# Performance work log

Measured on AMD Instinct MI355X. Metric: run time of the kernel, lower is better.

The kernel has to match this reference:

```python
import jax, jax.numpy as jnp
import numpy as np

N_NODES = 100000
N_EDGES = 400000
N_REL = 3
N_LAYERS = 2
D = 128          # input feature dim == hidden_dim so weights stack cleanly
N_CLASSES = 2


def setup_inputs() -> dict:
    key = jax.random.key(0)
    ks = jax.random.split(key, 7)
    x = jax.random.normal(ks[0], (N_NODES, D), dtype=jnp.float32)
    edge_index = jax.random.randint(ks[1], (N_REL, 2, N_EDGES), 0, N_NODES, dtype=jnp.int32)
    # SAGEConv params per (layer, relation): neighbor weight, root weight, bias
    Wn = jax.random.normal(ks[2], (N_LAYERS, N_REL, D, D), dtype=jnp.float32) * (1.0 / np.sqrt(D))
    Wr = jax.random.normal(ks[3], (N_LAYERS, N_REL, D, D), dtype=jnp.float32) * (1.0 / np.sqrt(D))
    b = jax.random.normal(ks[4], (N_LAYERS, N_REL, D), dtype=jnp.float32) * 0.02
    Wc = jax.random.normal(ks[5], (D, N_CLASSES), dtype=jnp.float32) * (1.0 / np.sqrt(D))
    bc = jax.random.normal(ks[6], (N_CLASSES,), dtype=jnp.float32) * 0.02
    return {"x": x, "edge_index": edge_index, "Wn": Wn, "Wr": Wr, "b": b, "Wc": Wc, "bc": bc}


def _mean_agg(h, ei, n_nodes):
    # gather source features, scatter-mean into destination nodes
    src, dst = ei[0], ei[1]
    s = jax.ops.segment_sum(h[src], dst, num_segments=n_nodes)          # [N, D]
    cnt = jax.ops.segment_sum(jnp.ones((ei.shape[1],), h.dtype), dst, num_segments=n_nodes)
    return s / jnp.maximum(cnt, 1.0)[:, None]


def reference(x, edge_index, Wn, Wr, b, Wc, bc):
    n = x.shape[0]
    h = x
    L, R = Wn.shape[0], Wn.shape[1]
    for l in range(L):
        out = jnp.zeros((n, Wn.shape[-1]), h.dtype)
        for r in range(R):
            # SAGEConv: lin_l(mean neighbors) + lin_r(root) + bias; HeteroConv sums relations
            agg = _mean_agg(h, edge_index[r], n)
            out = out + agg @ Wn[l, r] + h @ Wr[l, r] + b[l, r]
        h = jax.nn.relu(out) if l < L - 1 else out  # dropout is eval-mode identity
    return h @ Wc + bc
```

## Files before the change

kernel.cpp:

```cpp
#include <hip/hip_runtime.h>

#define NN 100000
#define NE 400000
#define NR 3
#define DD 128
#define NROWS (NR * NN)
#define NEDGES (NR * NE)
#define SCAN_BLOCKS ((NROWS + 1023) / 1024)

typedef float f32x4 __attribute__((ext_vector_type(4)));
typedef __bf16 bf16x8 __attribute__((ext_vector_type(8)));

__device__ __forceinline__ unsigned short f2bf(float f) {
    unsigned int u = __float_as_uint(f);
    u += 0x7fff + ((u >> 16) & 1);
    return (unsigned short)(u >> 16);
}

__device__ __forceinline__ void gload16(const void* g, void* l) {
    __builtin_amdgcn_global_load_lds(
        (const __attribute__((address_space(1))) void*)g,
        (__attribute__((address_space(3))) void*)l, 16, 0, 0);
}

__global__ __launch_bounds__(256) void cvt_x(const float* __restrict__ x,
                                             unsigned short* __restrict__ xb) {
    int i = blockIdx.x * 256 + threadIdx.x;
    const float4* xf = reinterpret_cast<const float4*>(x + (size_t)i * 8);
    float4 a = xf[0], b = xf[1];
    uint4 o;
    o.x = (unsigned)f2bf(a.x) | ((unsigned)f2bf(a.y) << 16);
    o.y = (unsigned)f2bf(a.z) | ((unsigned)f2bf(a.w) << 16);
    o.z = (unsigned)f2bf(b.x) | ((unsigned)f2bf(b.y) << 16);
    o.w = (unsigned)f2bf(b.z) | ((unsigned)f2bf(b.w) << 16);
    reinterpret_cast<uint4*>(xb)[i] = o;
}

__global__ __launch_bounds__(256) void prep_w(const float* __restrict__ Wn,
                                              const float* __restrict__ Wr,
                                              unsigned short* __restrict__ Wt) {
    int t = blockIdx.x * 256 + threadIdx.x;
    if (t >= 2 * 128 * 512) return;
    int l = t >> 16;
    int rem = t & 65535;
    int n = rem >> 9;
    int k = rem & 511;
    int rk = k >> 7, kk = k & 127;
    float v;
    if (rk < 3) {
        v = Wn[(((size_t)l * 3 + rk) * 128 + kk) * 128 + n];
    } else {
        const float* WrL = Wr + (size_t)l * 3 * 128 * 128;
        v = WrL[kk * 128 + n] + WrL[128 * 128 + kk * 128 + n] + WrL[2 * 128 * 128 + kk * 128 + n];
    }
    Wt[((size_t)l * 128 + n) * 512 + k] = f2bf(v);
}

__global__ __launch_bounds__(256) void prep_b(const float* __restrict__ b,
                                              float* __restrict__ bias) {
    int t = threadIdx.x;
    int l = t >> 7, n = t & 127;
    bias[t] = b[l * 384 + n] + b[l * 384 + 128 + n] + b[l * 384 + 256 + n];
}

__global__ __launch_bounds__(256) void csr_count(const int* __restrict__ ei,
                                                 int* __restrict__ cnt) {
    int t = blockIdx.x * 256 + threadIdx.x;
    if (t >= NEDGES) return;
    int r = t / NE;
    int e = t - r * NE;
    int dst = ei[(r * 2 + 1) * NE + e];
    atomicAdd(&cnt[r * NN + dst], 1);
}

__global__ __launch_bounds__(256) void scan1(const int* __restrict__ cnt,
                                             int* __restrict__ row_start,
                                             int* __restrict__ bsum) {
    __shared__ int sh[256];
    int b0 = blockIdx.x * 1024;
    int t = threadIdx.x;
    int v[4];
    int s = 0;
    #pragma unroll
    for (int j = 0; j < 4; ++j) {
        int idx = b0 + t * 4 + j;
        v[j] = (idx < NROWS) ? cnt[idx] : 0;
        s += v[j];
    }
    sh[t] = s;
    __syncthreads();
    for (int off = 1; off < 256; off <<= 1) {
        int val = (t >= off) ? sh[t - off] : 0;
        __syncthreads();
        sh[t] += val;
        __syncthreads();
    }
    int excl = (t == 0) ? 0 : sh[t - 1];
    if (t == 255) bsum[blockIdx.x] = sh[255];
    #pragma unroll
    for (int j = 0; j < 4; ++j) {
        int idx = b0 + t * 4 + j;
        if (idx < NROWS) { row_start[idx] = excl; excl += v[j]; }
    }
}

__global__ __launch_bounds__(512) void scan2(int* __restrict__ bsum, int nb) {
    __shared__ int sh[512];
    int t = threadIdx.x;
    sh[t] = (t < nb) ? bsum[t] : 0;
    __syncthreads();
    for (int off = 1; off < 512; off <<= 1) {
        int val = (t >= off) ? sh[t - off] : 0;
        __syncthreads();
        sh[t] += val;
        __syncthreads();
    }
    int excl = (t == 0) ? 0 : sh[t - 1];
    if (t < nb) bsum[t] = excl;
}

__global__ __launch_bounds__(256) void scan3(int* __restrict__ row_start,
                                             const int* __restrict__ bsum) {
    int idx = blockIdx.x * 256 + threadIdx.x;
    if (idx < NROWS) row_start[idx] += bsum[idx >> 10];
}

__global__ __launch_bounds__(256) void csr_fill(const int* __restrict__ ei,
                                                const int* __restrict__ row_start,
                                                int* __restrict__ cursor,
                                                int* __restrict__ bucket) {
    int t = blockIdx.x * 256 + threadIdx.x;
    if (t >= NEDGES) return;
    int r = t / NE;
    int e = t - r * NE;
    int src = ei[(r * 2 + 0) * NE + e];
    int dst = ei[(r * 2 + 1) * NE + e];
    int i = r * NN + dst;
    int pos = row_start[i] + atomicAdd(&cursor[i], 1);
    bucket[pos] = src;
}

__global__ __launch_bounds__(256) void gnn_gather(const unsigned short* __restrict__ h,
                                                  const int* __restrict__ bucket,
                                                  const int* __restrict__ row_start,
                                                  const int* __restrict__ cnt,
                                                  unsigned short* __restrict__ agg) {
    int wid = (blockIdx.x * 256 + threadIdx.x) >> 6;
    int lane = threadIdx.x & 63;
    if (wid >= NROWS) return;
    int base = row_start[wid];
    int deg = cnt[wid];
    const unsigned int* hw = reinterpret_cast<const unsigned int*>(h);
    float a0 = 0.f, a1 = 0.f, b0 = 0.f, b1 = 0.f;
    float c0 = 0.f, c1 = 0.f, d0 = 0.f, d1 = 0.f;
    int e = 0;
    for (; e + 4 <= deg; e += 4) {
        int s0 = bucket[base + e + 0];
        int s1 = bucket[base + e + 1];
        int s2 = bucket[base + e + 2];
        int s3 = bucket[base + e + 3];
        unsigned int v0 = hw[(size_t)s0 * 64 + lane];
        unsigned int v1 = hw[(size_t)s1 * 64 + lane];
        unsigned int v2 = hw[(size_t)s2 * 64 + lane];
        unsigned int v3 = hw[(size_t)s3 * 64 + lane];
        a0 += __uint_as_float(v0 << 16); a1 += __uint_as_float(v0 & 0xffff0000u);
        b0 += __uint_as_float(v1 << 16); b1 += __uint_as_float(v1 & 0xffff0000u);
        c0 += __uint_as_float(v2 << 16); c1 += __uint_as_float(v2 & 0xffff0000u);
        d0 += __uint_as_float(v3 << 16); d1 += __uint_as_float(v3 & 0xffff0000u);
    }
    for (; e < deg; ++e) {
        int s0 = bucket[base + e];
        unsigned int v0 = hw[(size_t)s0 * 64 + lane];
        a0 += __uint_as_float(v0 << 16); a1 += __uint_as_float(v0 & 0xffff0000u);
    }
    a0 = (a0 + b0) + (c0 + d0);
    a1 = (a1 + b1) + (c1 + d1);
    float sc = (deg > 0) ? (1.0f / (float)deg) : 0.0f;
    a0 *= sc; a1 *= sc;
    unsigned int o = (unsigned)f2bf(a0) | ((unsigned)f2bf(a1) << 16);
    reinterpret_cast<unsigned int*>(agg + (size_t)wid * DD)[lane] = o;
}

template <int RELU>
__global__ __launch_bounds__(256) void gemm_mfma(
    const unsigned short* __restrict__ aggb,
    const unsigned short* __restrict__ hb,
    const unsigned short* __restrict__ Wt,
    const float* __restrict__ bias,
    unsigned short* __restrict__ outb)
{
    __shared__ __align__(16) unsigned short As[2 * 128 * 32];
    __shared__ __align__(16) unsigned short Bs[2 * 128 * 32];
    const int t = threadIdx.x;
    const int w = t >> 6, lane = t & 63;
    const int m0 = blockIdx.x * 128;
    const int wr = w >> 1, wc = w & 1;
    const int fr = lane & 15;
    const int fq = lane >> 4;
    f32x4 acc[4][4] = {};

    auto stage = [&](int s, int buf) {
        const int srcid = s >> 2;
        const int k0 = (s & 3) * 32;
        const unsigned short* Asrc = (srcid < 3) ? (aggb + (size_t)srcid * NN * DD) : hb;
        #pragma unroll
        for (int i = 0; i < 2; ++i) {
            int row = i * 64 + w * 16 + (lane >> 2);
            int grow = m0 + row;
            if (grow > NN - 1) grow = NN - 1;
            const unsigned short* gA = Asrc + (size_t)grow * DD + k0 + (lane & 3) * 8;
            gload16(gA, (char*)As + buf * 8192 + i * 4096 + w * 1024);
            const unsigned short* gB = Wt + (size_t)row * 512 + srcid * 128 + k0 + (lane & 3) * 8;
            gload16(gB, (char*)Bs + buf * 8192 + i * 4096 + w * 1024);
        }
    };

    stage(0, 0);
    #pragma unroll
    for (int s = 0; s < 16; ++s) {
        const int cur = s & 1;
        __syncthreads();
        if (s + 1 < 16) stage(s + 1, cur ^ 1);
        bf16x8 af[4], bfr[4];
        #pragma unroll
        for (int m = 0; m < 4; ++m)
            af[m] = *reinterpret_cast<const bf16x8*>(As + cur * 4096 + (wr * 64 + m * 16 + fr) * 32 + fq * 8);
        #pragma unroll
        for (int n = 0; n < 4; ++n)
            bfr[n] = *reinterpret_cast<const bf16x8*>(Bs + cur * 4096 + (wc * 64 + n * 16 + fr) * 32 + fq * 8);
        #pragma unroll
        for (int m = 0; m < 4; ++m)
            #pragma unroll
            for (int n = 0; n < 4; ++n)
                acc[m][n] = __builtin_amdgcn_mfma_f32_16x16x32_bf16(af[m], bfr[n], acc[m][n], 0, 0, 0);
    }

    #pragma unroll
    for (int n = 0; n < 4; ++n) {
        int col = wc * 64 + n * 16 + fr;
        float bs = bias[col];
        #pragma unroll
        for (int m = 0; m < 4; ++m) {
            int rbase = m0 + wr * 64 + m * 16 + fq * 4;
            #pragma unroll
            for (int j = 0; j < 4; ++j) {
                int row = rbase + j;
                if (row < NN) {
                    float v = acc[m][n][j] + bs;
                    if (RELU) v = fmaxf(v, 0.f);
                    outb[(size_t)row * DD + col] = f2bf(v);
                }
            }
        }
    }
}

__global__ __launch_bounds__(256) void classify(const unsigned short* __restrict__ h2,
                                                const float* __restrict__ Wc,
                                                const float* __restrict__ bc,
                                                float* __restrict__ out) {
    int wid = (blockIdx.x * 256 + threadIdx.x) >> 6;
    int lane = threadIdx.x & 63;
    if (wid >= NN) return;
    float4 wc4 = reinterpret_cast<const float4*>(Wc)[lane];
    unsigned int v = reinterpret_cast<const unsigned int*>(h2 + (size_t)wid * DD)[lane];
    float v0 = __uint_as_float(v << 16);
    float v1 = __uint_as_float(v & 0xffff0000u);
    float p0 = v0 * wc4.x + v1 * wc4.z;
    float p1 = v0 * wc4.y + v1 * wc4.w;
    #pragma unroll
    for (int off = 1; off < 64; off <<= 1) {
        p0 += __shfl_xor(p0, off);
        p1 += __shfl_xor(p1, off);
    }
    if (lane == 0) {
        out[(size_t)wid * 2 + 0] = p0 + bc[0];
        out[(size_t)wid * 2 + 1] = p1 + bc[1];
    }
}

extern "C" void kernel_launch(void* const* d_in, const int* in_sizes, int n_in,
                              void* d_out, int out_size, void* d_ws, size_t ws_size,
                              hipStream_t stream) {
    const float* x  = (const float*)d_in[0];
    const int*   ei = (const int*)d_in[1];
    const float* Wn = (const float*)d_in[2];
    const float* Wr = (const float*)d_in[3];
    const float* b  = (const float*)d_in[4];
    const float* Wc = (const float*)d_in[5];
    const float* bc = (const float*)d_in[6];
    float* out = (float*)d_out;

    char* p = (char*)d_ws;
    unsigned short* aggb = (unsigned short*)p;  p += (size_t)NR * NN * DD * 2;
    unsigned short* xb   = (unsigned short*)p;  p += (size_t)NN * DD * 2;
    unsigned short* h1b  = (unsigned short*)p;  p += (size_t)NN * DD * 2;
    unsigned short* h2b  = (unsigned short*)p;  p += (size_t)NN * DD * 2;
    unsigned short* Wt   = (unsigned short*)p;  p += (size_t)2 * 128 * 512 * 2;
    float* bias          = (float*)p;           p += 2 * 128 * 4;
    int* bucket          = (int*)p;             p += (size_t)NEDGES * 4;
    int* cnt             = (int*)p;             p += (size_t)NROWS * 4;
    int* row_start       = (int*)p;             p += (size_t)NROWS * 4;
    int* cursor          = (int*)p;             p += (size_t)NROWS * 4;
    int* bsum            = (int*)p;             p += 512 * 4;

    hipMemsetAsync(cnt, 0, NROWS * sizeof(int), stream);
    hipMemsetAsync(cursor, 0, NROWS * sizeof(int), stream);

    csr_count<<<(NEDGES + 255) / 256, 256, 0, stream>>>(ei, cnt);
    scan1<<<SCAN_BLOCKS, 256, 0, stream>>>(cnt, row_start, bsum);
    scan2<<<1, 512, 0, stream>>>(bsum, SCAN_BLOCKS);
    scan3<<<(NROWS + 255) / 256, 256, 0, stream>>>(row_start, bsum);
    csr_fill<<<(NEDGES + 255) / 256, 256, 0, stream>>>(ei, row_start, cursor, bucket);

    cvt_x<<<(NN * DD / 8 + 255) / 256, 256, 0, stream>>>(x, xb);
    prep_w<<<(2 * 128 * 512 + 255) / 256, 256, 0, stream>>>(Wn, Wr, Wt);
    prep_b<<<1, 256, 0, stream>>>(b, bias);

    const int gatherBlocks = (NROWS * 64) / 256;
    const int gemmBlocks = (NN + 127) / 128;

    gnn_gather<<<gatherBlocks, 256, 0, stream>>>(xb, bucket, row_start, cnt, aggb);
    gemm_mfma<1><<<gemmBlocks, 256, 0, stream>>>(aggb, xb, Wt, bias, h1b);

    gnn_gather<<<gatherBlocks, 256, 0, stream>>>(h1b, bucket, row_start, cnt, aggb);
    gemm_mfma<0><<<gemmBlocks, 256, 0, stream>>>(aggb, h1b, Wt + (size_t)128 * 512,
                                                 bias + 128, h2b);

    classify<<<(NN * 64 + 255) / 256, 256, 0, stream>>>(h2b, Wc, bc, out);
}
```

Before: 518.2 us.

## Fuse prep kernels, fold scan3, prescale gather indices, drop GEMM LDS staging

```diff
diff --git a/kernel.cpp b/kernel.cpp
--- a/kernel.cpp
+++ b/kernel.cpp
@@ -15,12 +15,6 @@
     unsigned int u = __float_as_uint(f);
     u += 0x7fff + ((u >> 16) & 1);
     return (unsigned short)(u >> 16);
-}
-
-__device__ __forceinline__ void gload16(const void* g, void* l) {
-    __builtin_amdgcn_global_load_lds(
-        (const __attribute__((address_space(1))) void*)g,
-        (__attribute__((address_space(3))) void*)l, 16, 0, 0);
 }
 
 __global__ __launch_bounds__(256) void cvt_x(const float* __restrict__ x,
@@ -36,31 +30,31 @@
     reinterpret_cast<uint4*>(xb)[i] = o;
 }
 
-__global__ __launch_bounds__(256) void prep_w(const float* __restrict__ Wn,
-                                              const float* __restrict__ Wr,
-                                              unsigned short* __restrict__ Wt) {
+__global__ __launch_bounds__(256) void prep_wb(const float* __restrict__ Wn,
+                                               const float* __restrict__ Wr,
+                                               const float* __restrict__ b,
+                                               unsigned short* __restrict__ Wt,
+                                               float* __restrict__ bias) {
     int t = blockIdx.x * 256 + threadIdx.x;
-    if (t >= 2 * 128 * 512) return;
-    int l = t >> 16;
-    int rem = t & 65535;
-    int n = rem >> 9;
-    int k = rem & 511;
-    int rk = k >> 7, kk = k & 127;
-    float v;
-    if (rk < 3) {
-        v = Wn[(((size_t)l * 3 + rk) * 128 + kk) * 128 + n];
-    } else {
-        const float* WrL = Wr + (size_t)l * 3 * 128 * 128;
-        v = WrL[kk * 128 + n] + WrL[128 * 128 + kk * 128 + n] + WrL[2 * 128 * 128 + kk * 128 + n];
-    }
-    Wt[((size_t)l * 128 + n) * 512 + k] = f2bf(v);
-}
-
-__global__ __launch_bounds__(256) void prep_b(const float* __restrict__ b,
-                                              float* __restrict__ bias) {
-    int t = threadIdx.x;
-    int l = t >> 7, n = t & 127;
-    bias[t] = b[l * 384 + n] + b[l * 384 + 128 + n] + b[l * 384 + 256 + n];
+    if (t < 2 * 128 * 512) {
+        int l = t >> 16;
+        int rem = t & 65535;
+        int n = rem >> 9;
+        int k = rem & 511;
+        int rk = k >> 7, kk = k & 127;
+        float v;
+        if (rk < 3) {
+            v = Wn[(((size_t)l * 3 + rk) * 128 + kk) * 128 + n];
+        } else {
+            const float* WrL = Wr + (size_t)l * 3 * 128 * 128;
+            v = WrL[kk * 128 + n] + WrL[128 * 128 + kk * 128 + n] + WrL[2 * 128 * 128 + kk * 128 + n];
+        }
+        Wt[((size_t)l * 128 + n) * 512 + k] = f2bf(v);
+    } else if (t < 2 * 128 * 512 + 256) {
+        int tt = t - 2 * 128 * 512;
+        int l = tt >> 7, n = tt & 127;
+        bias[tt] = b[l * 384 + n] + b[l * 384 + 128 + n] + b[l * 384 + 256 + n];
+    }
 }
 
 __global__ __launch_bounds__(256) void csr_count(const int* __restrict__ ei,
@@ -119,14 +113,9 @@
     if (t < nb) bsum[t] = excl;
 }
 
-__global__ __launch_bounds__(256) void scan3(int* __restrict__ row_start,
-                                             const int* __restrict__ bsum) {
-    int idx = blockIdx.x * 256 + threadIdx.x;
-    if (idx < NROWS) row_start[idx] += bsum[idx >> 10];
-}
-
 __global__ __launch_bounds__(256) void csr_fill(const int* __restrict__ ei,
                                                 const int* __restrict__ row_start,
+                                                const int* __restrict__ bsum,
                                                 int* __restrict__ cursor,
                                                 int* __restrict__ bucket) {
     int t = blockIdx.x * 256 + threadIdx.x;
@@ -136,41 +125,69 @@
     int src = ei[(r * 2 + 0) * NE + e];
     int dst = ei[(r * 2 + 1) * NE + e];
     int i = r * NN + dst;
-    int pos = row_start[i] + atomicAdd(&cursor[i], 1);
-    bucket[pos] = src;
+    int pos = row_start[i] + bsum[i >> 10] + atomicAdd(&cursor[i], 1);
+    bucket[pos] = src << 8;
 }
 
 __global__ __launch_bounds__(256) void gnn_gather(const unsigned short* __restrict__ h,
                                                   const int* __restrict__ bucket,
                                                   const int* __restrict__ row_start,
+                                                  const int* __restrict__ bsum,
                                                   const int* __restrict__ cnt,
                                                   unsigned short* __restrict__ agg) {
     int wid = (blockIdx.x * 256 + threadIdx.x) >> 6;
     int lane = threadIdx.x & 63;
     if (wid >= NROWS) return;
-    int base = row_start[wid];
+    int base = row_start[wid] + bsum[wid >> 10];
     int deg = cnt[wid];
-    const unsigned int* hw = reinterpret_cast<const unsigned int*>(h);
+    const char* hb = (const char*)h;
+    const unsigned int lo = lane * 4;
     float a0 = 0.f, a1 = 0.f, b0 = 0.f, b1 = 0.f;
     float c0 = 0.f, c1 = 0.f, d0 = 0.f, d1 = 0.f;
     int e = 0;
-    for (; e + 4 <= deg; e += 4) {
-        int s0 = bucket[base + e + 0];
-        int s1 = bucket[base + e + 1];
-        int s2 = bucket[base + e + 2];
-        int s3 = bucket[base + e + 3];
-        unsigned int v0 = hw[(size_t)s0 * 64 + lane];
-        unsigned int v1 = hw[(size_t)s1 * 64 + lane];
-        unsigned int v2 = hw[(size_t)s2 * 64 + lane];
-        unsigned int v3 = hw[(size_t)s3 * 64 + lane];
+    for (; e + 8 <= deg; e += 8) {
+        unsigned int o0 = (unsigned)bucket[base + e + 0] + lo;
+        unsigned int o1 = (unsigned)bucket[base + e + 1] + lo;
+        unsigned int o2 = (unsigned)bucket[base + e + 2] + lo;
+        unsigned int o3 = (unsigned)bucket[base + e + 3] + lo;
+        unsigned int o4 = (unsigned)bucket[base + e + 4] + lo;
+        unsigned int o5 = (unsigned)bucket[base + e + 5] + lo;
+        unsigned int o6 = (unsigned)bucket[base + e + 6] + lo;
+        unsigned int o7 = (unsigned)bucket[base + e + 7] + lo;
+        unsigned int v0 = *(const unsigned int*)(hb + o0);
+        unsigned int v1 = *(const unsigned int*)(hb + o1);
+        unsigned int v2 = *(const unsigned int*)(hb + o2);
+        unsigned int v3 = *(const unsigned int*)(hb + o3);
+        unsigned int v4 = *(const unsigned int*)(hb + o4);
+        unsigned int v5 = *(const unsigned int*)(hb + o5);
+        unsigned int v6 = *(const unsigned int*)(hb + o6);
+        unsigned int v7 = *(const unsigned int*)(hb + o7);
         a0 += __uint_as_float(v0 << 16); a1 += __uint_as_float(v0 & 0xffff0000u);
         b0 += __uint_as_float(v1 << 16); b1 += __uint_as_float(v1 & 0xffff0000u);
         c0 += __uint_as_float(v2 << 16); c1 += __uint_as_float(v2 & 0xffff0000u);
         d0 += __uint_as_float(v3 << 16); d1 += __uint_as_float(v3 & 0xffff0000u);
+        a0 += __uint_as_float(v4 << 16); a1 += __uint_as_float(v4 & 0xffff0000u);
+        b0 += __uint_as_float(v5 << 16); b1 += __uint_as_float(v5 & 0xffff0000u);
+        c0 += __uint_as_float(v6 << 16); c1 += __uint_as_float(v6 & 0xffff0000u);
+        d0 += __uint_as_float(v7 << 16); d1 += __uint_as_float(v7 & 0xffff0000u);
+    }
+    for (; e + 4 <= deg; e += 4) {
+        unsigned int o0 = (unsigned)bucket[base + e + 0] + lo;
+        unsigned int o1 = (unsigned)bucket[base + e + 1] + lo;
+        unsigned int o2 = (unsigned)bucket[base + e + 2] + lo;
+        unsigned int o3 = (unsigned)bucket[base + e + 3] + lo;
+        unsigned int v0 = *(const unsigned int*)(hb + o0);
+        unsigned int v1 = *(const unsigned int*)(hb + o1);
+        unsigned int v2 = *(const unsigned int*)(hb + o2);
+        unsigned int v3 = *(const unsigned int*)(hb + o3);
+        a0 += __uint_as_float(v0 << 16); a1 += __uint_as_float(v0 & 0xffff0000u);
+        b0 += __uint_as_float(v1 << 16); b1 += __uint_as_float(v1 & 0xffff0000u);
+        c0 += __uint_as_float(v2 << 16); c1 += __uint_as_float(v2 & 0xffff0000u);
+        d0 += __uint_as_float(v3 << 16); d1 += __uint_as_float(v3 & 0xffff0000u);
     }
     for (; e < deg; ++e) {
-        int s0 = bucket[base + e];
-        unsigned int v0 = hw[(size_t)s0 * 64 + lane];
+        unsigned int o0 = (unsigned)bucket[base + e] + lo;
+        unsigned int v0 = *(const unsigned int*)(hb + o0);
         a0 += __uint_as_float(v0 << 16); a1 += __uint_as_float(v0 & 0xffff0000u);
     }
     a0 = (a0 + b0) + (c0 + d0);
@@ -182,15 +199,13 @@
 }
 
 template <int RELU>
-__global__ __launch_bounds__(256) void gemm_mfma(
+__global__ __launch_bounds__(256, 2) void gemm_mfma(
     const unsigned short* __restrict__ aggb,
     const unsigned short* __restrict__ hb,
     const unsigned short* __restrict__ Wt,
     const float* __restrict__ bias,
     unsigned short* __restrict__ outb)
 {
-    __shared__ __align__(16) unsigned short As[2 * 128 * 32];
-    __shared__ __align__(16) unsigned short Bs[2 * 128 * 32];
     const int t = threadIdx.x;
     const int w = t >> 6, lane = t & 63;
     const int m0 = blockIdx.x * 128;
@@ -199,35 +214,26 @@
     const int fq = lane >> 4;
     f32x4 acc[4][4] = {};
 
-    auto stage = [&](int s, int buf) {
+    int arow[4];
+    #pragma unroll
+    for (int m = 0; m < 4; ++m) {
+        int r = m0 + wr * 64 + m * 16 + fr;
+        arow[m] = (r > NN - 1) ? (NN - 1) : r;
+    }
+
+    #pragma unroll
+    for (int s = 0; s < 16; ++s) {
         const int srcid = s >> 2;
-        const int k0 = (s & 3) * 32;
+        const int kl = (s & 3) * 32 + fq * 8;
         const unsigned short* Asrc = (srcid < 3) ? (aggb + (size_t)srcid * NN * DD) : hb;
-        #pragma unroll
-        for (int i = 0; i < 2; ++i) {
-            int row = i * 64 + w * 16 + (lane >> 2);
-            int grow = m0 + row;
-            if (grow > NN - 1) grow = NN - 1;
-            const unsigned short* gA = Asrc + (size_t)grow * DD + k0 + (lane & 3) * 8;
-            gload16(gA, (char*)As + buf * 8192 + i * 4096 + w * 1024);
-            const unsigned short* gB = Wt + (size_t)row * 512 + srcid * 128 + k0 + (lane & 3) * 8;
-            gload16(gB, (char*)Bs + buf * 8192 + i * 4096 + w * 1024);
-        }
-    };
-
-    stage(0, 0);
-    #pragma unroll
-    for (int s = 0; s < 16; ++s) {
-        const int cur = s & 1;
-        __syncthreads();
-        if (s + 1 < 16) stage(s + 1, cur ^ 1);
+        const int kg = srcid * 128 + kl;
         bf16x8 af[4], bfr[4];
         #pragma unroll
         for (int m = 0; m < 4; ++m)
-            af[m] = *reinterpret_cast<const bf16x8*>(As + cur * 4096 + (wr * 64 + m * 16 + fr) * 32 + fq * 8);
+            af[m] = *reinterpret_cast<const bf16x8*>(Asrc + (size_t)arow[m] * DD + kl);
         #pragma unroll
         for (int n = 0; n < 4; ++n)
-            bfr[n] = *reinterpret_cast<const bf16x8*>(Bs + cur * 4096 + (wc * 64 + n * 16 + fr) * 32 + fq * 8);
+            bfr[n] = *reinterpret_cast<const bf16x8*>(Wt + (size_t)(wc * 64 + n * 16 + fr) * 512 + kg);
         #pragma unroll
         for (int m = 0; m < 4; ++m)
             #pragma unroll
@@ -310,20 +316,18 @@
     csr_count<<<(NEDGES + 255) / 256, 256, 0, stream>>>(ei, cnt);
     scan1<<<SCAN_BLOCKS, 256, 0, stream>>>(cnt, row_start, bsum);
     scan2<<<1, 512, 0, stream>>>(bsum, SCAN_BLOCKS);
-    scan3<<<(NROWS + 255) / 256, 256, 0, stream>>>(row_start, bsum);
-    csr_fill<<<(NEDGES + 255) / 256, 256, 0, stream>>>(ei, row_start, cursor, bucket);
+    csr_fill<<<(NEDGES + 255) / 256, 256, 0, stream>>>(ei, row_start, bsum, cursor, bucket);
 
     cvt_x<<<(NN * DD / 8 + 255) / 256, 256, 0, stream>>>(x, xb);
-    prep_w<<<(2 * 128 * 512 + 255) / 256, 256, 0, stream>>>(Wn, Wr, Wt);
-    prep_b<<<1, 256, 0, stream>>>(b, bias);
+    prep_wb<<<(2 * 128 * 512 + 256 + 255) / 256, 256, 0, stream>>>(Wn, Wr, b, Wt, bias);
 
     const int gatherBlocks = (NROWS * 64) / 256;
     const int gemmBlocks = (NN + 127) / 128;
 
-    gnn_gather<<<gatherBlocks, 256, 0, stream>>>(xb, bucket, row_start, cnt, aggb);
+    gnn_gather<<<gatherBlocks, 256, 0, stream>>>(xb, bucket, row_start, bsum, cnt, aggb);
     gemm_mfma<1><<<gemmBlocks, 256, 0, stream>>>(aggb, xb, Wt, bias, h1b);
 
-    gnn_gather<<<gatherBlocks, 256, 0, stream>>>(h1b, bucket, row_start, cnt, aggb);
+    gnn_gather<<<gatherBlocks, 256, 0, stream>>>(h1b, bucket, row_start, bsum, cnt, aggb);
     gemm_mfma<0><<<gemmBlocks, 256, 0, stream>>>(aggb, h1b, Wt + (size_t)128 * 512,
                                                  bias + 128, h2b);
 
```

Result: slower. 576.0 us (+11.1%).
